# Kernel tuning notes

Measured on AMD Instinct MI355X. Metric: run time of the kernel, lower is better.

## Reference

```python
import jax, jax.numpy as jnp
import numpy as np

N = 512          # num_atoms (sqrt of number of pairwise edges)
H = 512          # h_nf / in_edge_nf
T_STEPS = 100    # recon.total_time
K_RANK = 3       # coord_dims / low-rank k
POWER_STEPS = 10


def setup_inputs() -> dict:
    key = jax.random.key(0)
    ks = jax.random.split(key, 6)
    s = 1.0 / np.sqrt(H)
    return {
        "gnn_edge_out": jax.random.normal(ks[0], (N * N, H), jnp.float32),
        "W1": jax.random.normal(ks[1], (H, H), jnp.float32) * s,   # edge_mlp1 Linear
        "b1": jnp.zeros((H,), jnp.float32),
        "W2": jax.random.normal(ks[2], (H, 2), jnp.float32) * s,    # edge_mlp2 Linear(h_nf, edge_out_nf=2)
        "b2": jnp.zeros((2,), jnp.float32),
        "noise_x": jax.random.normal(ks[3], (N, K_RANK), jnp.float32),  # randn added to low-rank init
        "u_init": jax.random.normal(ks[4], (N, K_RANK), jnp.float32),   # power-iteration random starts
    }


def reference(gnn_edge_out, W1, b1, W2, b2, noise_x, u_init):
    # ---- DistWeightLayer ----
    h = jax.nn.relu(gnn_edge_out @ W1 + b1)          # edge_mlp1 (MLP, 1 layer)
    emb = jnp.sum(h)[None]                           # sum over dims (0,1), unsqueeze -> (1,)
    e = jax.nn.softplus(h @ W2 + b2)                 # (N*N, 2) softplus(edge_mlp2)
    D_init = e[:, 0].reshape(N, N) * (1.0 - jnp.eye(N, dtype=e.dtype))
    W = e[:, 1].reshape(N, N)

    # ---- dist_to_gram ----
    D = D_init
    D_row = jnp.mean(D, axis=0)                      # (N,)
    D_col = jnp.mean(D, axis=1, keepdims=True)       # (N,1)
    D_mean = jnp.mean(D)
    B = -0.5 * (D - D_row - D_col + D_mean)

    # ---- low_rank_approx_power (k=3, deflation) ----
    A_lr = B
    us = []
    for i in range(K_RANK):
        u = u_init[:, i:i + 1]                       # (N,1)
        for _ in range(POWER_STEPS):
            u = u / jnp.maximum(jnp.linalg.norm(u), 1e-3)  # F.normalize eps=0.001
            u = A_lr @ u
        eig_sq = jnp.sum(u * u)
        u = u * (eig_sq + 0.01) ** 0.25              # u / pow(eig_sq+0.01, -0.25)
        us.append(u)
        A_lr = A_lr - u @ u.T
    X = jnp.concatenate(us, axis=1) + noise_x        # (N,3)

    # ---- 100-step distance-geometry descent (step_func) ----
    def U_fn(Xc):
        diff = Xc[:, None, :] - Xc[None, :, :]       # (N,N,3)
        Dx = jnp.sqrt(jnp.sum(diff * diff, axis=-1) + 0.01)  # tsg_eps
        return jnp.sum(W * jnp.square(D_init - Dx))

    def step(Xc, t):
        g = jax.grad(U_fn)(Xc)
        dX = -0.1 * g                                # tsg_eps1
        speed = jnp.sqrt(jnp.sum(dX * dX, axis=-1, keepdims=True) + 0.001)  # tsg_eps2
        alpha_t = 0.1 + (5.0 - 0.1) * (T_STEPS - t) / T_STEPS
        scale = alpha_t * jnp.tanh(speed / alpha_t) / speed
        return Xc + dX * scale, None

    X_pred, _ = jax.lax.scan(step, X, jnp.arange(T_STEPS, dtype=X.dtype))
    return (D_init, W, emb, X_pred)
```

## Files before the change

kernel.cpp:

```cpp
#include <hip/hip_runtime.h>
#include <hip/hip_bf16.h>
#include <math.h>

#define NN 512
#define ROWS (NN * NN)
#define HH 512

#define NB 16
#define NT 512
#define RPB 32

#define WS_EMB   0
#define WS_COLP  4096
#define WS_U0    (WS_COLP + 32*512)
#define WS_U1    (WS_U0 + 512)
#define WS_X0    (WS_U1 + 512)
#define WS_X1    (WS_X0 + 2048)
#define WS_W1F   (WS_X1 + 2048)
#define WS_BAR   (WS_W1F + 131072)

typedef __attribute__((ext_vector_type(8))) short bf16x8;
typedef __attribute__((ext_vector_type(4))) float f32x4;

#define AGENT __HIP_MEMORY_SCOPE_AGENT

__device__ __forceinline__ short f2bf(float f) {
    union { float f; unsigned u; } v; v.f = f;
    unsigned r = v.u + 0x7fffu + ((v.u >> 16) & 1u);
    return (short)(r >> 16);
}

__device__ __forceinline__ unsigned pack_bf2(float lo, float hi) {
    return __builtin_amdgcn_perm(__float_as_uint(hi), __float_as_uint(lo),
                                 0x07060302u);
}

__device__ __forceinline__ float softplus_f(float x) {
    return fmaxf(x, 0.0f) + log1pf(expf(-fabsf(x)));
}

__device__ __forceinline__ unsigned long long pk64(float a, float b) {
    return ((unsigned long long)__float_as_uint(b) << 32) |
           (unsigned long long)__float_as_uint(a);
}

__global__ void w1f_prep(const float* __restrict__ W1, short* __restrict__ W1F)
{
    const int c = blockIdx.x * 256 + threadIdx.x;
    const int lane = c & 63;
    const int g = c >> 6;
    const int colg = g & 31;
    const int kc = g >> 5;
    const int col = colg * 16 + (lane & 15);
    const int kb = kc * 32 + (lane >> 4) * 8;
    bf16x8 w;
    #pragma unroll
    for (int j = 0; j < 8; j++)
        w[j] = f2bf(W1[(size_t)(kb + j) * HH + col]);
    *(bf16x8*)(W1F + (size_t)c * 8) = w;
}

__global__ __launch_bounds__(512, 4) void fused_mlp(
    const float* __restrict__ A, const short* __restrict__ W1F,
    const float* __restrict__ b1, const float* __restrict__ W2,
    const float* __restrict__ b2, float* __restrict__ outD,
    float* __restrict__ outW, float* __restrict__ embpart)
{
    __shared__ short As[2][64 * 40];
    __shared__ float sp0[8][64], sp1[8][64];
    __shared__ float semb[8];

    const int tid = threadIdx.x;
    const int lane = tid & 63;
    const int wc = tid >> 6;
    const int l15 = lane & 15;
    const int l4 = lane >> 4;
    const int row0 = blockIdx.x * 64;

    f32x4 acc[4][4];
    #pragma unroll
    for (int m = 0; m < 4; m++)
        #pragma unroll
        for (int n = 0; n < 4; n++) {
            f32x4 z = {0.0f, 0.0f, 0.0f, 0.0f};
            acc[m][n] = z;
        }

    const int sr = tid >> 3;
    const int sk4 = (tid & 7) * 4;
    const float* agp = A + (size_t)(row0 + sr) * HH + sk4;

    const short* bfp = W1F + ((size_t)(wc * 4) * 64 + lane) * 8;

    {
        float4 a0 = *(const float4*)agp;
        uint2 w = {pack_bf2(a0.x, a0.y), pack_bf2(a0.z, a0.w)};
        *(uint2*)&As[0][sr * 40 + sk4] = w;
    }
    __syncthreads();

    int cur = 0;
    #pragma unroll 1
    for (int s = 0; s < 16; s++) {
        const int k0 = s * 32;
        bf16x8 bfr[4];
        #pragma unroll
        for (int n = 0; n < 4; n++)
            bfr[n] = *(const bf16x8*)(bfp + s * 16384 + n * 512);
        float4 pv;
        if (s < 15) pv = *(const float4*)(agp + k0 + 32);
        bf16x8 af[4];
        #pragma unroll
        for (int m = 0; m < 4; m++)
            af[m] = *(const bf16x8*)&As[cur][(m * 16 + l15) * 40 + l4 * 8];
        #pragma unroll
        for (int m = 0; m < 4; m++)
            #pragma unroll
            for (int n = 0; n < 4; n++)
                acc[m][n] = __builtin_amdgcn_mfma_f32_16x16x32_bf16(
                    af[m], bfr[n], acc[m][n], 0, 0, 0);
        if (s < 15) {
            uint2 w = {pack_bf2(pv.x, pv.y), pack_bf2(pv.z, pv.w)};
            *(uint2*)&As[cur ^ 1][sr * 40 + sk4] = w;
        }
        __syncthreads();
        cur ^= 1;
    }

    float b1c[4], w20[4], w21[4];
    #pragma unroll
    for (int n = 0; n < 4; n++) {
        int col = wc * 64 + n * 16 + l15;
        b1c[n] = b1[col];
        w20[n] = W2[col * 2 + 0];
        w21[n] = W2[col * 2 + 1];
    }
    float embl = 0.0f;
    #pragma unroll
    for (int m = 0; m < 4; m++) {
        #pragma unroll
        for (int j = 0; j < 4; j++) {
            float s0 = 0.0f, s1 = 0.0f;
            #pragma unroll
            for (int n = 0; n < 4; n++) {
                float h = fmaxf(acc[m][n][j] + b1c[n], 0.0f);
                s0 = fmaf(h, w20[n], s0);
                s1 = fmaf(h, w21[n], s1);
                embl += h;
            }
            #pragma unroll
            for (int st = 1; st < 16; st <<= 1) {
                s0 += __shfl_xor(s0, st);
                s1 += __shfl_xor(s1, st);
            }
            if (l15 == 0) {
                int row = m * 16 + l4 * 4 + j;
                sp0[wc][row] = s0;
                sp1[wc][row] = s1;
            }
        }
    }
    #pragma unroll
    for (int st = 1; st < 64; st <<= 1) embl += __shfl_xor(embl, st);
    if (lane == 0) semb[wc] = embl;
    __syncthreads();
    if (tid < 64) {
        int gr = row0 + tid;
        float p0 = b2[0], p1 = b2[1];
        #pragma unroll
        for (int w = 0; w < 8; w++) { p0 += sp0[w][tid]; p1 += sp1[w][tid]; }
        int di = gr >> 9, dj = gr & 511;
        outD[gr] = (di == dj) ? 0.0f : softplus_f(p0);
        outW[gr] = softplus_f(p1);
    }
    if (tid == 0) {
        float e = 0.0f;
        #pragma unroll
        for (int w = 0; w < 8; w++) e += semb[w];
        embpart[blockIdx.x] = e;
    }
}

__device__ __forceinline__ void gbar(int* cnt, int target)
{
    __syncthreads();
    if (threadIdx.x == 0)
        __hip_atomic_fetch_add(cnt, 1, __ATOMIC_RELAXED, AGENT);
    if (threadIdx.x < 64) {
        while (__hip_atomic_load(cnt, __ATOMIC_RELAXED, AGENT) < target)
            __builtin_amdgcn_s_sleep(1);
    }
    __syncthreads();
}

__device__ __forceinline__ void block_sum5(float* v, float (*red)[8], int tid) {
    #pragma unroll
    for (int s = 1; s < 64; s <<= 1)
        #pragma unroll
        for (int q = 0; q < 5; q++) v[q] += __shfl_xor(v[q], s);
    if ((tid & 63) == 0)
        #pragma unroll
        for (int q = 0; q < 5; q++) red[q][tid >> 6] = v[q];
    __syncthreads();
    #pragma unroll
    for (int q = 0; q < 5; q++) {
        float r = 0.0f;
        #pragma unroll
        for (int i = 0; i < 8; i++) r += red[q][i];
        v[q] = r;
    }
    __syncthreads();
}

__device__ __forceinline__ float block_sum1(float v, float (*red)[8], int tid) {
    #pragma unroll
    for (int s = 1; s < 64; s <<= 1) v += __shfl_xor(v, s);
    if ((tid & 63) == 0) red[0][tid >> 6] = v;
    __syncthreads();
    float r = 0.0f;
    #pragma unroll
    for (int i = 0; i < 8; i++) r += red[0][i];
    __syncthreads();
    return r;
}

__global__ __launch_bounds__(512, 1) void coop_post(
    const float* __restrict__ Dg, const float* __restrict__ Wg,
    const float* __restrict__ noise, const float* __restrict__ uinit,
    float* __restrict__ outE, float* __restrict__ outX,
    float* __restrict__ ws)
{
    __shared__ float Dl[RPB][516];
    __shared__ float S1[RPB][516];
    __shared__ float Xl[512][4];
    __shared__ float ul[512];
    __shared__ float upl[3][512];
    __shared__ float cm[512];
    __shared__ float rm[RPB];
    __shared__ float red5[5][8];

    const int tid = threadIdx.x;
    const int bid = blockIdx.x;
    const int r0 = bid * RPB;

    float* embpart = ws + WS_EMB;
    float* colpart = ws + WS_COLP;
    float* ubuf0   = ws + WS_U0;
    float* ubuf1   = ws + WS_U1;
    float* Xg0     = ws + WS_X0;
    float* Xg1     = ws + WS_X1;
    int* cnt       = (int*)(ws + WS_BAR);
    int bg = 0;

    for (int idx = tid; idx < RPB * 512; idx += NT) {
        int r = idx >> 9, c = idx & 511;
        Dl[r][c] = Dg[(size_t)(r0 + r) * NN + c];
    }
    __syncthreads();
    const int mr = tid >> 4;
    const int ml = tid & 15;
    {
        float s = 0.0f;
        for (int j = ml; j < 512; j += 16) s += Dl[mr][j];
        #pragma unroll
        for (int st = 1; st < 16; st <<= 1) s += __shfl_xor(s, st);
        if (ml == 0) rm[mr] = s * (1.0f / 512.0f);
    }
    {
        float s = 0.0f;
        #pragma unroll
        for (int r = 0; r < RPB; r++) s += Dl[r][tid];
        __hip_atomic_store(&colpart[bid * 512 + tid], s, __ATOMIC_RELAXED, AGENT);
    }
    gbar(cnt, NB * ++bg);

    {
        float s = 0.0f;
        #pragma unroll
        for (int p = 0; p < NB; p++)
            s += __hip_atomic_load(&colpart[p * 512 + tid], __ATOMIC_RELAXED, AGENT);
        cm[tid] = s * (1.0f / 512.0f);
    }
    if (bid == 0) {
        float s = 0.0f;
        for (int i = tid; i < ROWS / 64; i += NT) s += embpart[i];
        s = block_sum1(s, red5, tid);
        if (tid == 0) outE[0] = s;
    }
    __syncthreads();
    float Dmean = block_sum1(cm[tid], red5, tid) * (1.0f / 512.0f);

    int cur = 0;
    #pragma unroll 1
    for (int rank = 0; rank < 3; rank++) {
        #pragma unroll 1
        for (int step = 0; step < 10; step++) {
            if (step == 0) {
                ul[tid] = uinit[tid * 3 + rank];
            } else {
                const float* ub = cur ? ubuf1 : ubuf0;
                ul[tid] = __hip_atomic_load(&ub[tid], __ATOMIC_RELAXED, AGENT);
            }
            __syncthreads();
            float u = ul[tid];
            float v[5];
            v[0] = u * u;
            v[1] = u;
            v[2] = cm[tid] * u;
            v[3] = (rank > 0) ? upl[0][tid] * u : 0.0f;
            v[4] = (rank > 1) ? upl[1][tid] * u : 0.0f;
            block_sum5(v, red5, tid);
            float inv = 1.0f / fmaxf(sqrtf(v[0]), 0.001f);
            float S = v[1] * inv, dr = v[2] * inv;
            float d0s = v[3] * inv, d1s = v[4] * inv;
            float a = 0.0f;
            for (int j = ml; j < 512; j += 16) a = fmaf(Dl[mr][j], ul[j], a);
            #pragma unroll
            for (int st = 1; st < 16; st <<= 1) a += __shfl_xor(a, st);
            if (ml == 0) {
                float bvv = -0.5f * (a * inv - dr - rm[mr] * S + Dmean * S);
                if (rank > 0) bvv -= d0s * upl[0][r0 + mr];
                if (rank > 1) bvv -= d1s * upl[1][r0 + mr];
                float* ubn = cur ? ubuf0 : ubuf1;
                __hip_atomic_store(&ubn[r0 + mr], bvv, __ATOMIC_RELAXED, AGENT);
            }
            gbar(cnt, NB * ++bg);
            cur ^= 1;
        }
        {
            const float* ub = cur ? ubuf1 : ubuf0;
            float u = __hip_atomic_load(&ub[tid], __ATOMIC_RELAXED, AGENT);
            float eig2 = block_sum1(u * u, red5, tid);
            float scl = sqrtf(sqrtf(eig2 + 0.01f));
            upl[rank][tid] = u * scl;
            Xl[tid][rank] = fmaf(u, scl, noise[tid * 3 + rank]);
            if (rank == 0) Xl[tid][3] = 0.0f;
            __syncthreads();
        }
    }

    for (int idx = tid; idx < RPB * 512; idx += NT) {
        int r = idx >> 9, j = idx & 511;
        int gr = r0 + r;
        float wr = Wg[(size_t)gr * NN + j];
        float wc = Wg[(size_t)j * NN + gr];
        float dc = Dg[(size_t)j * NN + gr];
        float d  = Dl[r][j];
        S1[r][j] = wr + wc;
        Dl[r][j] = fmaf(wr, d, wc * dc);
    }
    __syncthreads();

    unsigned long long* X064 = (unsigned long long*)Xg0;
    unsigned long long* X164 = (unsigned long long*)Xg1;
    int par = 0;
    #pragma unroll 1
    for (int t = 0; t < 100; t++) {
        float xr0 = Xl[r0 + mr][0], xr1 = Xl[r0 + mr][1], xr2 = Xl[r0 + mr][2];
        float g0 = 0, g1 = 0, g2 = 0;
        for (int j = ml; j < 512; j += 16) {
            float dx0 = xr0 - Xl[j][0];
            float dx1 = xr1 - Xl[j][1];
            float dx2 = xr2 - Xl[j][2];
            float d2 = fmaf(dx0, dx0, fmaf(dx1, dx1, fmaf(dx2, dx2, 0.01f)));
            float ri = rsqrtf(d2);
            float coef = fmaf(Dl[mr][j], ri, -S1[mr][j]);
            g0 = fmaf(coef, dx0, g0);
            g1 = fmaf(coef, dx1, g1);
            g2 = fmaf(coef, dx2, g2);
        }
        #pragma unroll
        for (int st = 1; st < 16; st <<= 1) {
            g0 += __shfl_xor(g0, st);
            g1 += __shfl_xor(g1, st);
            g2 += __shfl_xor(g2, st);
        }
        if (ml == 0) {
            float dX0 = 0.2f * g0, dX1 = 0.2f * g1, dX2 = 0.2f * g2;
            float sp = sqrtf(fmaf(dX0, dX0, fmaf(dX1, dX1, fmaf(dX2, dX2, 0.001f))));
            float alpha = 0.1f + 4.9f * (float)(100 - t) * 0.01f;
            float scal = alpha * tanhf(sp / alpha) / sp;
            float n0 = fmaf(dX0, scal, xr0);
            float n1 = fmaf(dX1, scal, xr1);
            float n2 = fmaf(dX2, scal, xr2);
            int gr = r0 + mr;
            if (t == 99) {
                outX[gr * 3 + 0] = n0;
                outX[gr * 3 + 1] = n1;
                outX[gr * 3 + 2] = n2;
            } else {
                unsigned long long* Xd64 = par ? X164 : X064;
                __hip_atomic_store(&Xd64[gr * 2], pk64(n0, n1),
                                   __ATOMIC_RELAXED, AGENT);
                __hip_atomic_store(&Xd64[gr * 2 + 1], pk64(n2, 0.0f),
                                   __ATOMIC_RELAXED, AGENT);
            }
        }
        if (t == 99) break;
        gbar(cnt, NB * ++bg);
        {
            const unsigned long long* Xs64 = par ? X164 : X064;
            unsigned long long lo =
                __hip_atomic_load(&Xs64[tid * 2], __ATOMIC_RELAXED, AGENT);
            unsigned long long hi =
                __hip_atomic_load(&Xs64[tid * 2 + 1], __ATOMIC_RELAXED, AGENT);
            Xl[tid][0] = __uint_as_float((unsigned)lo);
            Xl[tid][1] = __uint_as_float((unsigned)(lo >> 32));
            Xl[tid][2] = __uint_as_float((unsigned)hi);
            Xl[tid][3] = 0.0f;
        }
        __syncthreads();
        par ^= 1;
    }
}

extern "C" void kernel_launch(void* const* d_in, const int* in_sizes, int n_in,
                              void* d_out, int out_size, void* d_ws, size_t ws_size,
                              hipStream_t stream)
{
    const float* A     = (const float*)d_in[0];
    const float* W1    = (const float*)d_in[1];
    const float* b1    = (const float*)d_in[2];
    const float* W2    = (const float*)d_in[3];
    const float* b2    = (const float*)d_in[4];
    const float* noise = (const float*)d_in[5];
    const float* uinit = (const float*)d_in[6];

    float* out  = (float*)d_out;
    float* outD = out;
    float* outW = out + ROWS;
    float* outE = out + 2 * ROWS;
    float* outX = out + 2 * ROWS + 1;
    float* ws   = (float*)d_ws;
    short* W1F  = (short*)(ws + WS_W1F);

    (void)hipMemsetAsync((char*)d_ws + (size_t)WS_BAR * sizeof(float), 0,
                         512 * sizeof(int), stream);

    hipLaunchKernelGGL(w1f_prep, dim3(128), dim3(256), 0, stream, W1, W1F);

    hipLaunchKernelGGL(fused_mlp, dim3(ROWS / 64), dim3(512), 0, stream,
                       A, W1F, b1, W2, b2, outD, outW, ws + WS_EMB);

    const float* Dg  = outD;
    const float* Wgc = outW;
    void* args[] = { (void*)&Dg, (void*)&Wgc, (void*)&noise, (void*)&uinit,
                     (void*)&outE, (void*)&outX, (void*)&ws };
    (void)hipLaunchCooperativeKernel((const void*)coop_post, dim3(NB), dim3(NT),
                                     args, 0, stream);
}
```

Before: 863.7 us.

## Halve cooperative blocks, pack descent coefficients as bf16, prefetch GEMM A tiles deeper

The cooperative post-processing kernel now runs on 8 blocks of 1024 threads, each owning 64 rows, instead of 16 blocks of 512 threads. This cuts the number of grid-barrier participants. To fit 64 rows in LDS, the two descent coefficient matrices (W sums and W·D sums) are packed as bf16 pairs into the single D buffer, which lowers precision of the gradient coefficients. Separately, the GEMM kernel prefetches the A operand two k-steps ahead and replaces __syncthreads with an explicit lgkmcnt wait plus s_barrier.

Result: slower. 1.133 ms (+31.2%).

```diff
diff --git a/kernel.cpp b/kernel.cpp
--- a/kernel.cpp
+++ b/kernel.cpp
@@ -6,9 +6,9 @@
 #define ROWS (NN * NN)
 #define HH 512
 
-#define NB 16
-#define NT 512
-#define RPB 32
+#define NB 8
+#define NT 1024
+#define RPB 64
 
 #define WS_EMB   0
 #define WS_COLP  4096
@@ -97,18 +97,18 @@
         uint2 w = {pack_bf2(a0.x, a0.y), pack_bf2(a0.z, a0.w)};
         *(uint2*)&As[0][sr * 40 + sk4] = w;
     }
+    float4 pvA = *(const float4*)(agp + 32);
     __syncthreads();
 
     int cur = 0;
     #pragma unroll 1
     for (int s = 0; s < 16; s++) {
-        const int k0 = s * 32;
+        float4 pvB = pvA;
+        if (s < 14) pvB = *(const float4*)(agp + s * 32 + 64);
         bf16x8 bfr[4];
         #pragma unroll
         for (int n = 0; n < 4; n++)
             bfr[n] = *(const bf16x8*)(bfp + s * 16384 + n * 512);
-        float4 pv;
-        if (s < 15) pv = *(const float4*)(agp + k0 + 32);
         bf16x8 af[4];
         #pragma unroll
         for (int m = 0; m < 4; m++)
@@ -120,10 +120,12 @@
                 acc[m][n] = __builtin_amdgcn_mfma_f32_16x16x32_bf16(
                     af[m], bfr[n], acc[m][n], 0, 0, 0);
         if (s < 15) {
-            uint2 w = {pack_bf2(pv.x, pv.y), pack_bf2(pv.z, pv.w)};
+            uint2 w = {pack_bf2(pvA.x, pvA.y), pack_bf2(pvA.z, pvA.w)};
             *(uint2*)&As[cur ^ 1][sr * 40 + sk4] = w;
         }
-        __syncthreads();
+        asm volatile("s_waitcnt lgkmcnt(0)" ::: "memory");
+        __builtin_amdgcn_s_barrier();
+        pvA = pvB;
         cur ^= 1;
     }
 
@@ -193,7 +195,7 @@
     __syncthreads();
 }
 
-__device__ __forceinline__ void block_sum5(float* v, float (*red)[8], int tid) {
+__device__ __forceinline__ void block_sum5(float* v, float (*red)[16], int tid) {
     #pragma unroll
     for (int s = 1; s < 64; s <<= 1)
         #pragma unroll
@@ -206,38 +208,37 @@
     for (int q = 0; q < 5; q++) {
         float r = 0.0f;
         #pragma unroll
-        for (int i = 0; i < 8; i++) r += red[q][i];
+        for (int i = 0; i < 16; i++) r += red[q][i];
         v[q] = r;
     }
     __syncthreads();
 }
 
-__device__ __forceinline__ float block_sum1(float v, float (*red)[8], int tid) {
+__device__ __forceinline__ float block_sum1(float v, float (*red)[16], int tid) {
     #pragma unroll
     for (int s = 1; s < 64; s <<= 1) v += __shfl_xor(v, s);
     if ((tid & 63) == 0) red[0][tid >> 6] = v;
     __syncthreads();
     float r = 0.0f;
     #pragma unroll
-    for (int i = 0; i < 8; i++) r += red[0][i];
+    for (int i = 0; i < 16; i++) r += red[0][i];
     __syncthreads();
     return r;
 }
 
-__global__ __launch_bounds__(512, 1) void coop_post(
+__global__ __launch_bounds__(NT, 1) void coop_post(
     const float* __restrict__ Dg, const float* __restrict__ Wg,
     const float* __restrict__ noise, const float* __restrict__ uinit,
     float* __restrict__ outE, float* __restrict__ outX,
     float* __restrict__ ws)
 {
-    __shared__ float Dl[RPB][516];
-    __shared__ float S1[RPB][516];
+    __shared__ float Dbuf[RPB][520];
     __shared__ float Xl[512][4];
     __shared__ float ul[512];
     __shared__ float upl[3][512];
     __shared__ float cm[512];
     __shared__ float rm[RPB];
-    __shared__ float red5[5][8];
+    __shared__ float red5[5][16];
 
     const int tid = threadIdx.x;
     const int bid = blockIdx.x;
@@ -254,27 +255,27 @@
 
     for (int idx = tid; idx < RPB * 512; idx += NT) {
         int r = idx >> 9, c = idx & 511;
-        Dl[r][c] = Dg[(size_t)(r0 + r) * NN + c];
+        Dbuf[r][c] = Dg[(size_t)(r0 + r) * NN + c];
     }
     __syncthreads();
     const int mr = tid >> 4;
     const int ml = tid & 15;
     {
         float s = 0.0f;
-        for (int j = ml; j < 512; j += 16) s += Dl[mr][j];
+        for (int j = ml; j < 512; j += 16) s += Dbuf[mr][j];
         #pragma unroll
         for (int st = 1; st < 16; st <<= 1) s += __shfl_xor(s, st);
         if (ml == 0) rm[mr] = s * (1.0f / 512.0f);
     }
-    {
+    if (tid < 512) {
         float s = 0.0f;
         #pragma unroll
-        for (int r = 0; r < RPB; r++) s += Dl[r][tid];
+        for (int r = 0; r < RPB; r++) s += Dbuf[r][tid];
         __hip_atomic_store(&colpart[bid * 512 + tid], s, __ATOMIC_RELAXED, AGENT);
     }
     gbar(cnt, NB * ++bg);
 
-    {
+    if (tid < 512) {
         float s = 0.0f;
         #pragma unroll
         for (int p = 0; p < NB; p++)
@@ -288,33 +289,42 @@
         if (tid == 0) outE[0] = s;
     }
     __syncthreads();
-    float Dmean = block_sum1(cm[tid], red5, tid) * (1.0f / 512.0f);
+    float Dmean;
+    {
+        float v = (tid < 512) ? cm[tid] : 0.0f;
+        Dmean = block_sum1(v, red5, tid) * (1.0f / 512.0f);
+    }
 
     int cur = 0;
     #pragma unroll 1
     for (int rank = 0; rank < 3; rank++) {
         #pragma unroll 1
         for (int step = 0; step < 10; step++) {
-            if (step == 0) {
-                ul[tid] = uinit[tid * 3 + rank];
-            } else {
-                const float* ub = cur ? ubuf1 : ubuf0;
-                ul[tid] = __hip_atomic_load(&ub[tid], __ATOMIC_RELAXED, AGENT);
+            if (tid < 512) {
+                if (step == 0) ul[tid] = uinit[tid * 3 + rank];
+                else {
+                    const float* ub = cur ? ubuf1 : ubuf0;
+                    ul[tid] = __hip_atomic_load(&ub[tid], __ATOMIC_RELAXED, AGENT);
+                }
             }
             __syncthreads();
-            float u = ul[tid];
+            float u = 0, cmv = 0, up0 = 0, up1 = 0;
+            if (tid < 512) {
+                u = ul[tid]; cmv = cm[tid];
+                up0 = upl[0][tid]; up1 = upl[1][tid];
+            }
             float v[5];
             v[0] = u * u;
             v[1] = u;
-            v[2] = cm[tid] * u;
-            v[3] = (rank > 0) ? upl[0][tid] * u : 0.0f;
-            v[4] = (rank > 1) ? upl[1][tid] * u : 0.0f;
+            v[2] = cmv * u;
+            v[3] = (rank > 0) ? up0 * u : 0.0f;
+            v[4] = (rank > 1) ? up1 * u : 0.0f;
             block_sum5(v, red5, tid);
             float inv = 1.0f / fmaxf(sqrtf(v[0]), 0.001f);
             float S = v[1] * inv, dr = v[2] * inv;
             float d0s = v[3] * inv, d1s = v[4] * inv;
             float a = 0.0f;
-            for (int j = ml; j < 512; j += 16) a = fmaf(Dl[mr][j], ul[j], a);
+            for (int j = ml; j < 512; j += 16) a = fmaf(Dbuf[mr][j], ul[j], a);
             #pragma unroll
             for (int st = 1; st < 16; st <<= 1) a += __shfl_xor(a, st);
             if (ml == 0) {
@@ -329,25 +339,33 @@
         }
         {
             const float* ub = cur ? ubuf1 : ubuf0;
-            float u = __hip_atomic_load(&ub[tid], __ATOMIC_RELAXED, AGENT);
+            float u = 0.0f;
+            if (tid < 512)
+                u = __hip_atomic_load(&ub[tid], __ATOMIC_RELAXED, AGENT);
             float eig2 = block_sum1(u * u, red5, tid);
             float scl = sqrtf(sqrtf(eig2 + 0.01f));
-            upl[rank][tid] = u * scl;
-            Xl[tid][rank] = fmaf(u, scl, noise[tid * 3 + rank]);
-            if (rank == 0) Xl[tid][3] = 0.0f;
+            if (tid < 512) {
+                upl[rank][tid] = u * scl;
+                Xl[tid][rank] = fmaf(u, scl, noise[tid * 3 + rank]);
+                if (rank == 0) Xl[tid][3] = 0.0f;
+            }
             __syncthreads();
         }
     }
 
-    for (int idx = tid; idx < RPB * 512; idx += NT) {
-        int r = idx >> 9, j = idx & 511;
+    #pragma unroll 1
+    for (int p = 0; p < RPB / 2; p++) {
+        int r = 2 * p + (tid >> 9);
+        int j = tid & 511;
         int gr = r0 + r;
+        float d  = Dbuf[r][j];
         float wr = Wg[(size_t)gr * NN + j];
-        float wc = Wg[(size_t)j * NN + gr];
+        float wcv = Wg[(size_t)j * NN + gr];
         float dc = Dg[(size_t)j * NN + gr];
-        float d  = Dl[r][j];
-        S1[r][j] = wr + wc;
-        Dl[r][j] = fmaf(wr, d, wc * dc);
+        float s1 = wr + wcv;
+        float s2 = fmaf(wr, d, wcv * dc);
+        __syncthreads();
+        *(unsigned*)&Dbuf[r][j] = pack_bf2(s1, s2);
     }
     __syncthreads();
 
@@ -357,6 +375,7 @@
     #pragma unroll 1
     for (int t = 0; t < 100; t++) {
         float xr0 = Xl[r0 + mr][0], xr1 = Xl[r0 + mr][1], xr2 = Xl[r0 + mr][2];
+        const unsigned* s12row = (const unsigned*)&Dbuf[mr][0];
         float g0 = 0, g1 = 0, g2 = 0;
         for (int j = ml; j < 512; j += 16) {
             float dx0 = xr0 - Xl[j][0];
@@ -364,7 +383,10 @@
             float dx2 = xr2 - Xl[j][2];
             float d2 = fmaf(dx0, dx0, fmaf(dx1, dx1, fmaf(dx2, dx2, 0.01f)));
             float ri = rsqrtf(d2);
-            float coef = fmaf(Dl[mr][j], ri, -S1[mr][j]);
+            unsigned pv = s12row[j];
+            float s1 = __uint_as_float(pv << 16);
+            float s2 = __uint_as_float(pv & 0xffff0000u);
+            float coef = fmaf(s2, ri, -s1);
             g0 = fmaf(coef, dx0, g0);
             g1 = fmaf(coef, dx1, g1);
             g2 = fmaf(coef, dx2, g2);
@@ -398,7 +420,7 @@
         }
         if (t == 99) break;
         gbar(cnt, NB * ++bg);
-        {
+        if (tid < 512) {
             const unsigned long long* Xs64 = par ? X164 : X064;
             unsigned long long lo =
                 __hip_atomic_load(&Xs64[tid * 2], __ATOMIC_RELAXED, AGENT);
```
